# Kernel tuning notes

Measured on AMD Instinct MI355X. Metric: run time of the kernel, lower is better.

## Reference

```python
import jax, jax.numpy as jnp
import numpy as np

TAU = 2.0   # spikingjelly LIFNode default tau
VTH = 1.0   # config.vthreshold

@jax.custom_vjp
def atan_spike(x):
    # heaviside forward, ATan surrogate backward (spikingjelly surrogate.ATan, alpha=2)
    return (x >= 0).astype(x.dtype)

def _atan_fwd(x):
    return atan_spike(x), x

def _atan_bwd(x, g):
    alpha = 2.0
    return (g * (alpha / 2.0) / (1.0 + (jnp.pi / 2.0 * alpha * x) ** 2),)

atan_spike.defvjp(_atan_fwd, _atan_bwd)

def layer_norm(x, eps=1e-6):
    m = jnp.mean(x, axis=-1, keepdims=True)
    v = jnp.mean((x - m) ** 2, axis=-1, keepdims=True)
    return (x - m) * jax.lax.rsqrt(v + eps)

def time_shift(x):
    # ZeroPad2d((0,0,1,-1)): xx[:, t] = x[:, t-1], xx[:, 0] = 0
    return jnp.pad(x, ((0, 0), (1, 0), (0, 0)))[:, :-1]

def lif_multistep(x4):
    # spikingjelly LIFNode, step_mode='m', decay_input=True, hard reset to v_reset=0
    def step(v, xt):
        v = v + (xt - v) / TAU
        s = atan_spike(v - VTH)
        return v * (1.0 - s), s
    _, spikes = jax.lax.scan(step, jnp.zeros_like(x4[0]), x4)
    return spikes

def wkv(w, u, k, v):
    # RWKV-v4 numerically-stable WKV scan. w: [C] (negative), u: [C], k,v: [B,T,C]
    B, T, C = k.shape
    def step(carry, kv):
        aa, bb, pp = carry
        kt, vt = kv
        ww = u + kt
        p = jnp.maximum(pp, ww)
        e1 = jnp.exp(pp - p); e2 = jnp.exp(ww - p)
        y = (e1 * aa + e2 * vt) / (e1 * bb + e2)
        ww2 = pp + w
        p2 = jnp.maximum(ww2, kt)
        f1 = jnp.exp(ww2 - p2); f2 = jnp.exp(kt - p2)
        return (f1 * aa + f2 * vt, f1 * bb + f2, p2), y
    init = (jnp.zeros((B, C), k.dtype), jnp.zeros((B, C), k.dtype),
            jnp.full((B, C), -1e38, k.dtype))
    _, ys = jax.lax.scan(step, init, (jnp.moveaxis(k, 1, 0), jnp.moveaxis(v, 1, 0)))
    return jnp.moveaxis(ys, 0, 1)

def time_mix(h, time_decay, time_first, tmk, tmv, tmr, Wk, Wv, Wr, Wo):
    xx = time_shift(h)
    xk = h * tmk + xx * (1 - tmk)
    xv = h * tmv + xx * (1 - tmv)
    xr = h * tmr + xx * (1 - tmr)
    k = jnp.einsum('btc,oc->bto', xk, Wk)
    v = jnp.einsum('btc,oc->bto', xv, Wv)
    sr = jax.nn.sigmoid(jnp.einsum('btc,oc->bto', xr, Wr))
    y = wkv(-jnp.exp(time_decay), time_first, k, v)
    return jnp.einsum('btc,oc->bto', sr * y, Wo)

def channel_mix(h, cmk, cmr, Wck, Wcv, Wcr):
    xx = time_shift(h)
    xk = h * cmk + xx * (1 - cmk)
    xr = h * cmr + xx * (1 - cmr)
    k = jnp.square(jax.nn.relu(jnp.einsum('btc,hc->bth', xk, Wck)))
    kv = jnp.einsum('bth,ch->btc', k, Wcv)
    return jax.nn.sigmoid(jnp.einsum('btc,oc->bto', xr, Wcr)) * kv

def _forward(x, rt, time_decay, time_first, tmix_k, tmix_v, tmix_r,
             Wk, Wv, Wr, Wo, cmix_k, cmix_r, Wck, Wcv, Wcr,
             Wrm, brm, Wam, bam):
    B, P1, C = x.shape
    xc = jnp.concatenate([x, jnp.broadcast_to(rt, (B, P1, C))], axis=1)  # [B, 2*P1, C]
    att = time_mix(layer_norm(xc), time_decay, time_first,
                   tmix_k, tmix_v, tmix_r, Wk, Wv, Wr, Wo)
    att = lif_multistep(jnp.broadcast_to(att, (4,) + att.shape)).mean(0)
    xc = xc + att
    ffn = channel_mix(layer_norm(xc), cmix_k, cmix_r, Wck, Wcv, Wcr)
    ffn = lif_multistep(jnp.broadcast_to(ffn, (4,) + ffn.shape)).mean(0)
    xc = xc + ffn
    xo, rtok = xc[:, :P1], xc[:, P1:]
    r = jnp.einsum('bpc,qc->bpq', rtok, Wrm) + brm   # restruction_token_MLP [B,P1,P1]
    r = jnp.swapaxes(r, 1, 2)                        # permute(0,2,1)
    r = jnp.einsum('bpq,cq->bpc', r, Wam) + bam      # another_MLP [B,P1,C]
    return xo + xo * r

def setup_inputs() -> dict:
    key = jax.random.key(0)
    ks = jax.random.split(key, 20)
    B, P1, C = 8, 256, 1024
    H = 4 * C
    s = 0.02
    f32 = jnp.float32
    return {
        'x': jax.random.normal(ks[0], (B, P1, C), f32),
        'rt': jax.random.normal(ks[1], (1, P1, C), f32) * 0.5,
        'time_decay': jax.random.normal(ks[2], (C,), f32),
        'time_first': jax.random.normal(ks[3], (C,), f32) * 0.3,
        'tmix_k': jax.random.uniform(ks[4], (1, 1, C), f32),
        'tmix_v': jax.random.uniform(ks[5], (1, 1, C), f32),
        'tmix_r': jax.random.uniform(ks[6], (1, 1, C), f32),
        'Wk': jax.random.normal(ks[7], (C, C), f32) * s,
        'Wv': jax.random.normal(ks[8], (C, C), f32) * s,
        'Wr': jax.random.normal(ks[9], (C, C), f32) * s,
        'Wo': jax.random.normal(ks[10], (C, C), f32) * s,
        'cmix_k': jax.random.uniform(ks[11], (1, 1, C), f32),
        'cmix_r': jax.random.uniform(ks[12], (1, 1, C), f32),
        'Wck': jax.random.normal(ks[13], (H, C), f32) * s,
        'Wcv': jax.random.normal(ks[14], (C, H), f32) * s,
        'Wcr': jax.random.normal(ks[15], (C, C), f32) * s,
        'Wrm': jax.random.normal(ks[16], (P1, C), f32) * s,
        'brm': jax.random.normal(ks[17], (P1,), f32) * s,
        'Wam': jax.random.normal(ks[18], (C, P1), f32) * s,
        'bam': jax.random.normal(ks[19], (C,), f32) * s,
    }

def reference(x, rt, time_decay, time_first, tmix_k, tmix_v, tmix_r,
              Wk, Wv, Wr, Wo, cmix_k, cmix_r, Wck, Wcv, Wcr,
              Wrm, brm, Wam, bam):
    return _forward(x, rt, time_decay, time_first, tmix_k, tmix_v, tmix_r,
                    Wk, Wv, Wr, Wo, cmix_k, cmix_r, Wck, Wcv, Wcr,
                    Wrm, brm, Wam, bam)
```

## Files before the change

### kernel.cpp

```cpp
#include <hip/hip_runtime.h>
#include <hip/hip_bf16.h>
#include <math.h>
#include <stdint.h>

#define TB_ 8
#define TT_ 512
#define TC_ 1024
#define WKV_NCH 32
#define WKV_L 16

typedef __attribute__((ext_vector_type(8))) short bf16x8;
typedef __attribute__((ext_vector_type(4))) short s16x4;
typedef __attribute__((ext_vector_type(4))) float f32x4;

__device__ __forceinline__ float b2f(short u) {
  union { unsigned int i; float f; } x;
  x.i = ((unsigned int)(unsigned short)u) << 16;
  return x.f;
}
__device__ __forceinline__ short f2b(float f) {
  __hip_bfloat16 h = __float2bfloat16(f);
  return __builtin_bit_cast(short, h);
}
__device__ __forceinline__ float sigm(float x) { return 1.0f / (1.0f + expf(-x)); }

__device__ __forceinline__ float lif4(float a) {
  float v = 0.0f, acc = 0.0f;
#pragma unroll
  for (int i = 0; i < 4; ++i) {
    v += (a - v) * 0.5f;
    float s = (v >= 1.0f) ? 1.0f : 0.0f;
    acc += s;
    v *= (1.0f - s);
  }
  return acc * 0.25f;
}

__device__ __forceinline__ void gload16(const void* g, void* l) {
  __builtin_amdgcn_global_load_lds(
      (__attribute__((address_space(1))) void*)(g),
      (__attribute__((address_space(3))) void*)(l), 16, 0, 0);
}

template <int N>
__device__ __forceinline__ void waitv() {
  if constexpr (N == 0)  asm volatile("s_waitcnt vmcnt(0)" ::: "memory");
  else if constexpr (N == 2)  asm volatile("s_waitcnt vmcnt(2)" ::: "memory");
  else if constexpr (N == 4)  asm volatile("s_waitcnt vmcnt(4)" ::: "memory");
  else if constexpr (N == 8)  asm volatile("s_waitcnt vmcnt(8)" ::: "memory");
  else if constexpr (N == 12) asm volatile("s_waitcnt vmcnt(12)" ::: "memory");
  else if constexpr (N == 16) asm volatile("s_waitcnt vmcnt(16)" ::: "memory");
  else if constexpr (N == 20) asm volatile("s_waitcnt vmcnt(20)" ::: "memory");
  else if constexpr (N == 24) asm volatile("s_waitcnt vmcnt(24)" ::: "memory");
  else if constexpr (N == 28) asm volatile("s_waitcnt vmcnt(28)" ::: "memory");
  else static_assert(N == 0, "unsupported vmcnt");
}
__device__ __forceinline__ void barrier_() {
  asm volatile("s_barrier" ::: "memory");
}


__global__ __launch_bounds__(256) void ln_mix3(
    const float* __restrict__ x, const float* __restrict__ rt,
    const float* __restrict__ tmk, const float* __restrict__ tmv,
    const float* __restrict__ tmr, float* __restrict__ xc,
    short* __restrict__ xk, short* __restrict__ xv, short* __restrict__ xr) {
  __shared__ float red[256];
  int row = blockIdx.x;
  int t = row & 511, b = row >> 9;
  int tid = threadIdx.x;
  const float* src = (t < 256) ? x + (int64_t)(b * 256 + t) * TC_
                               : rt + (int64_t)(t - 256) * TC_;
  float4 v = ((const float4*)src)[tid];
  ((float4*)(xc + (int64_t)row * TC_))[tid] = v;
  red[tid] = v.x + v.y + v.z + v.w;
  __syncthreads();
  for (int off = 128; off > 0; off >>= 1) {
    if (tid < off) red[tid] += red[tid + off];
    __syncthreads();
  }
  float mean = red[0] * (1.0f / 1024.0f);
  __syncthreads();
  float dx = v.x - mean, dy = v.y - mean, dz = v.z - mean, dw = v.w - mean;
  red[tid] = dx * dx + dy * dy + dz * dz + dw * dw;
  __syncthreads();
  for (int off = 128; off > 0; off >>= 1) {
    if (tid < off) red[tid] += red[tid + off];
    __syncthreads();
  }
  float rs = 1.0f / sqrtf(red[0] * (1.0f / 1024.0f) + 1e-6f);
  float c0 = dx * rs, c1 = dy * rs, c2 = dz * rs, c3 = dw * rs;
  float p0 = 0.f, p1 = 0.f, p2 = 0.f, p3 = 0.f;
  if (t > 0) {
    int tp = t - 1;
    const float* srcp = (tp < 256) ? x + (int64_t)(b * 256 + tp) * TC_
                                   : rt + (int64_t)(tp - 256) * TC_;
    __syncthreads();
    float4 w4 = ((const float4*)srcp)[tid];
    red[tid] = w4.x + w4.y + w4.z + w4.w;
    __syncthreads();
    for (int off = 128; off > 0; off >>= 1) {
      if (tid < off) red[tid] += red[tid + off];
      __syncthreads();
    }
    float meanp = red[0] * (1.0f / 1024.0f);
    __syncthreads();
    float ex = w4.x - meanp, ey = w4.y - meanp, ez = w4.z - meanp,
          ew = w4.w - meanp;
    red[tid] = ex * ex + ey * ey + ez * ez + ew * ew;
    __syncthreads();
    for (int off = 128; off > 0; off >>= 1) {
      if (tid < off) red[tid] += red[tid + off];
      __syncthreads();
    }
    float rsp = 1.0f / sqrtf(red[0] * (1.0f / 1024.0f) + 1e-6f);
    p0 = ex * rsp; p1 = ey * rsp; p2 = ez * rsp; p3 = ew * rsp;
  }
  int c = tid * 4;
  int64_t o = (int64_t)row * TC_ + c;
  float m0, m1, m2, m3;
  s16x4 ov;
  m0 = tmk[c]; m1 = tmk[c + 1]; m2 = tmk[c + 2]; m3 = tmk[c + 3];
  ov.x = f2b(c0 * m0 + p0 * (1.0f - m0));
  ov.y = f2b(c1 * m1 + p1 * (1.0f - m1));
  ov.z = f2b(c2 * m2 + p2 * (1.0f - m2));
  ov.w = f2b(c3 * m3 + p3 * (1.0f - m3));
  *(s16x4*)(xk + o) = ov;
  m0 = tmv[c]; m1 = tmv[c + 1]; m2 = tmv[c + 2]; m3 = tmv[c + 3];
  ov.x = f2b(c0 * m0 + p0 * (1.0f - m0));
  ov.y = f2b(c1 * m1 + p1 * (1.0f - m1));
  ov.z = f2b(c2 * m2 + p2 * (1.0f - m2));
  ov.w = f2b(c3 * m3 + p3 * (1.0f - m3));
  *(s16x4*)(xv + o) = ov;
  m0 = tmr[c]; m1 = tmr[c + 1]; m2 = tmr[c + 2]; m3 = tmr[c + 3];
  ov.x = f2b(c0 * m0 + p0 * (1.0f - m0));
  ov.y = f2b(c1 * m1 + p1 * (1.0f - m1));
  ov.z = f2b(c2 * m2 + p2 * (1.0f - m2));
  ov.w = f2b(c3 * m3 + p3 * (1.0f - m3));
  *(s16x4*)(xr + o) = ov;
}

__global__ __launch_bounds__(256) void ln_mix2(const float* __restrict__ xc,
                                               const float* __restrict__ cmk,
                                               const float* __restrict__ cmr,
                                               short* __restrict__ xk,
                                               short* __restrict__ xr) {
  __shared__ float red[256];
  int row = blockIdx.x;
  int t = row & 511;
  int tid = threadIdx.x;
  float4 v = ((const float4*)(xc + (int64_t)row * TC_))[tid];
  red[tid] = v.x + v.y + v.z + v.w;
  __syncthreads();
  for (int off = 128; off > 0; off >>= 1) {
    if (tid < off) red[tid] += red[tid + off];
    __syncthreads();
  }
  float mean = red[0] * (1.0f / 1024.0f);
  __syncthreads();
  float dx = v.x - mean, dy = v.y - mean, dz = v.z - mean, dw = v.w - mean;
  red[tid] = dx * dx + dy * dy + dz * dz + dw * dw;
  __syncthreads();
  for (int off = 128; off > 0; off >>= 1) {
    if (tid < off) red[tid] += red[tid + off];
    __syncthreads();
  }
  float rs = 1.0f / sqrtf(red[0] * (1.0f / 1024.0f) + 1e-6f);
  float c0 = dx * rs, c1 = dy * rs, c2 = dz * rs, c3 = dw * rs;
  float p0 = 0.f, p1 = 0.f, p2 = 0.f, p3 = 0.f;
  if (t > 0) {
    __syncthreads();
    float4 w4 = ((const float4*)(xc + (int64_t)(row - 1) * TC_))[tid];
    red[tid] = w4.x + w4.y + w4.z + w4.w;
    __syncthreads();
    for (int off = 128; off > 0; off >>= 1) {
      if (tid < off) red[tid] += red[tid + off];
      __syncthreads();
    }
    float meanp = red[0] * (1.0f / 1024.0f);
    __syncthreads();
    float ex = w4.x - meanp, ey = w4.y - meanp, ez = w4.z - meanp,
          ew = w4.w - meanp;
    red[tid] = ex * ex + ey * ey + ez * ez + ew * ew;
    __syncthreads();
    for (int off = 128; off > 0; off >>= 1) {
      if (tid < off) red[tid] += red[tid + off];
      __syncthreads();
    }
    float rsp = 1.0f / sqrtf(red[0] * (1.0f / 1024.0f) + 1e-6f);
    p0 = ex * rsp; p1 = ey * rsp; p2 = ez * rsp; p3 = ew * rsp;
  }
  int c = tid * 4;
  float k0 = cmk[c], k1 = cmk[c + 1], k2 = cmk[c + 2], k3 = cmk[c + 3];
  float r0 = cmr[c], r1 = cmr[c + 1], r2 = cmr[c + 2], r3 = cmr[c + 3];
  s16x4 ok, orr;
  ok.x = f2b(c0 * k0 + p0 * (1.0f - k0));
  ok.y = f2b(c1 * k1 + p1 * (1.0f - k1));
  ok.z = f2b(c2 * k2 + p2 * (1.0f - k2));
  ok.w = f2b(c3 * k3 + p3 * (1.0f - k3));
  orr.x = f2b(c0 * r0 + p0 * (1.0f - r0));
  orr.y = f2b(c1 * r1 + p1 * (1.0f - r1));
  orr.z = f2b(c2 * r2 + p2 * (1.0f - r2));
  orr.w = f2b(c3 * r3 + p3 * (1.0f - r3));
  *(s16x4*)(xk + (int64_t)row * TC_ + c) = ok;
  *(s16x4*)(xr + (int64_t)row * TC_ + c) = orr;
}

__global__ __launch_bounds__(256) void cvt_b(const float* __restrict__ src,
                                             short* __restrict__ dst) {
  int64_t i = (int64_t)(blockIdx.x * 256 + threadIdx.x) * 8;
  float4 a = *(const float4*)(src + i);
  float4 b = *(const float4*)(src + i + 4);
  bf16x8 o;
  o[0] = f2b(a.x); o[1] = f2b(a.y); o[2] = f2b(a.z); o[3] = f2b(a.w);
  o[4] = f2b(b.x); o[5] = f2b(b.y); o[6] = f2b(b.z); o[7] = f2b(b.w);
  *(bf16x8*)(dst + i) = o;
}

__global__ __launch_bounds__(256) void cvt_all(
    const float* __restrict__ Wk, const float* __restrict__ Wv,
    const float* __restrict__ Wr, const float* __restrict__ Wo,
    const float* __restrict__ Wcr, const float* __restrict__ Wcv,
    const float* __restrict__ Wrm, const float* __restrict__ Wam,
    short* __restrict__ bWk, short* __restrict__ bWv, short* __restrict__ bWr,
    short* __restrict__ bWo, short* __restrict__ bWcr, short* __restrict__ bWcv,
    short* __restrict__ bWrm, short* __restrict__ bWam,
    float* __restrict__ S) {
  int bid = blockIdx.x;
  if (bid >= 4864) {
    int row = (bid - 4864) * 4 + (threadIdx.x >> 6);
    int lane = threadIdx.x & 63;
    float4 v = ((const float4*)(Wam + (int64_t)row * 256))[lane];
    float s = v.x + v.y + v.z + v.w;
    for (int off = 32; off > 0; off >>= 1) s += __shfl_down(s, off);
    if (lane == 0) S[row] = s;
    return;
  }
  const float* src; short* dst; int base;
  if (bid < 512)       { src = Wk;  dst = bWk;  base = bid; }
  else if (bid < 1024) { src = Wv;  dst = bWv;  base = bid - 512; }
  else if (bid < 1536) { src = Wr;  dst = bWr;  base = bid - 1024; }
  else if (bid < 2048) { src = Wo;  dst = bWo;  base = bid - 1536; }
  else if (bid < 2560) { src = Wcr; dst = bWcr; base = bid - 2048; }
  else if (bid < 4608) { src = Wcv; dst = bWcv; base = bid - 2560; }
  else if (bid < 4736) { src = Wrm; dst = bWrm; base = bid - 4608; }
  else                 { src = Wam; dst = bWam; base = bid - 4736; }
  int64_t i = ((int64_t)base * 256 + threadIdx.x) * 8;
  float4 a = *(const float4*)(src + i);
  float4 b = *(const float4*)(src + i + 4);
  bf16x8 o;
  o[0] = f2b(a.x); o[1] = f2b(a.y); o[2] = f2b(a.z); o[3] = f2b(a.w);
  o[4] = f2b(b.x); o[5] = f2b(b.y); o[6] = f2b(b.z); o[7] = f2b(b.w);
  *(bf16x8*)(dst + i) = o;
}

__global__ __launch_bounds__(256) void wkv_p1(const float* __restrict__ td,
                                              const short* __restrict__ K,
                                              const short* __restrict__ V,
                                              float* __restrict__ Ca,
                                              float* __restrict__ Da,
                                              float* __restrict__ Qa) {
  int bx = blockIdx.x;
  int ch = bx >> 5;
  int b = (bx >> 2) & 7;
  int c = (bx & 3) * 256 + threadIdx.x;
  float w = -expf(td[c]);
  float aa = 0.0f, bb = 0.0f, pp = -1e38f;
  int64_t base = ((int64_t)b * TT_ + ch * WKV_L) * TC_ + c;
#pragma unroll
  for (int t = 0; t < WKV_L; ++t) {
    int64_t o = base + (int64_t)t * TC_;
    float kt = b2f(K[o]), vt = b2f(V[o]);
    float ww2 = pp + w;
    float p2 = fmaxf(ww2, kt);
    float e1 = expf(ww2 - p2);
    float e2 = expf(kt - p2);
    aa = e1 * aa + e2 * vt;
    bb = e1 * bb + e2;
    pp = p2;
  }
  int idx = ch * 8192 + b * 1024 + c;
  Ca[idx] = aa; Da[idx] = bb; Qa[idx] = pp;
}

__global__ __launch_bounds__(256) void wkv_p2(const float* __restrict__ td,
                                              const float* __restrict__ Ca,
                                              const float* __restrict__ Da,
                                              const float* __restrict__ Qa,
                                              float* __restrict__ Aa,
                                              float* __restrict__ Ba,
                                              float* __restrict__ Pa) {
  int i = blockIdx.x * 256 + threadIdx.x;
  int c = i & (TC_ - 1);
  float wL = -expf(td[c]) * (float)WKV_L;
  float aa = 0.0f, bb = 0.0f, pp = -1e38f;
#pragma unroll 4
  for (int ch = 0; ch < WKV_NCH; ++ch) {
    int idx = ch * 8192 + i;
    Aa[idx] = aa; Ba[idx] = bb; Pa[idx] = pp;
    float ppw = pp + wL;
    float q = Qa[idx];
    float p2 = fmaxf(ppw, q);
    float ea = expf(ppw - p2);
    float eb = expf(q - p2);
    aa = aa * ea + Ca[idx] * eb;
    bb = bb * ea + Da[idx] * eb;
    pp = p2;
  }
}

__global__ __launch_bounds__(256) void wkv_p3(const float* __restrict__ td,
                                              const float* __restrict__ tf,
                                              const short* __restrict__ K,
                                              const short* __restrict__ V,
                                              const short* __restrict__ SR,
                                              short* __restrict__ SRY,
                                              const float* __restrict__ Aa,
                                              const float* __restrict__ Ba,
                                              const float* __restrict__ Pa) {
  int bx = blockIdx.x;
  int ch = bx >> 5;
  int b = (bx >> 2) & 7;
  int c = (bx & 3) * 256 + threadIdx.x;
  float w = -expf(td[c]);
  float u = tf[c];
  int idx = ch * 8192 + b * 1024 + c;
  float aa = Aa[idx], bb = Ba[idx], pp = Pa[idx];
  int64_t base = ((int64_t)b * TT_ + ch * WKV_L) * TC_ + c;
#pragma unroll
  for (int t = 0; t < WKV_L; ++t) {
    int64_t o = base + (int64_t)t * TC_;
    float kt = b2f(K[o]), vt = b2f(V[o]);
    float ww = u + kt;
    float p = fmaxf(pp, ww);
    float E1 = expf(pp - p);
    float E2 = expf(ww - p);
    float y = (E1 * aa + E2 * vt) / (E1 * bb + E2);
    SRY[o] = f2b(y * b2f(SR[o]));
    float ww2 = pp + w;
    float p2 = fmaxf(ww2, kt);
    float e1 = expf(ww2 - p2);
    float e2 = expf(kt - p2);
    aa = e1 * aa + e2 * vt;
    bb = e1 * bb + e2;
    pp = p2;
  }
}

template <int BM, int BN, int EPI, int D, int MINW>
__global__ __launch_bounds__(256, MINW) void gemm_bf16(
    const short* __restrict__ A, const short* __restrict__ B,
    void* __restrict__ Cp, int M, int N, int K, int Kst,
    int64_t sA, int64_t sB, int64_t sC,
    const float* __restrict__ e0, const float* __restrict__ e1,
    const float* __restrict__ e2, const void* __restrict__ e3, int64_t sE) {
  constexpr int MF = BM / 32;
  constexpr int NF = BN / 32;
  constexpr int ASLOT = BM / 64;
  constexpr int BSLOT = BN / 64;
  constexpr int NL = ASLOT + BSLOT;
  constexpr int SBUF = (BM + BN) * 32;
  __shared__ short lds[D * SBUF];
  const int tid = threadIdx.x;

  const unsigned gx = gridDim.x, gy = gridDim.y;
  const unsigned nwg = gx * gy * gridDim.z;
  const unsigned lin = blockIdx.x + gx * (blockIdx.y + gy * blockIdx.z);
  const unsigned cs = nwg >> 3;
  const unsigned nl = (lin & 7) * cs + (lin >> 3);
  const unsigned bxs = nl % gx;
  const unsigned tmp = nl / gx;
  const unsigned bys = tmp % gy;
  const unsigned bz = tmp / gy;

  const int brow = bys * BM;
  const int bcol = bxs * BN;
  const short* Ab = A + bz * sA;
  const short* Bb = B + bz * sB;

  const int srow = ((tid >> 6) << 4) + (tid & 15);
  const int skc = ((tid >> 4) & 3) * 8;
  const short* gA[ASLOT];
  const short* gB[BSLOT];
#pragma unroll
  for (int s = 0; s < ASLOT; ++s)
    gA[s] = Ab + (int64_t)(brow + s * 64 + srow) * Kst + skc;
#pragma unroll
  for (int s = 0; s < BSLOT; ++s)
    gB[s] = Bb + (int64_t)(bcol + s * 64 + srow) * Kst + skc;

  const int lane = tid & 63, wid = tid >> 6;
  const int wr = wid >> 1, wc = wid & 1;

  f32x4 acc[MF][NF] = {};

  auto stage = [&](int buf, int k0) {
    short* d = lds + buf * SBUF;
#pragma unroll
    for (int s = 0; s < ASLOT; ++s)
      gload16(gA[s] + k0, d + s * 2048 + tid * 8);
#pragma unroll
    for (int s = 0; s < BSLOT; ++s)
      gload16(gB[s] + k0, d + BM * 32 + s * 2048 + tid * 8);
  };
  auto compute = [&](int buf) {
    const short* base = lds + buf * SBUF;
    bf16x8 af[MF], bfv[NF];
#pragma unroll
    for (int m = 0; m < MF; ++m)
      af[m] = *(const bf16x8*)(base + (wr * MF + m) * 512 + lane * 8);
#pragma unroll
    for (int n = 0; n < NF; ++n)
      bfv[n] = *(const bf16x8*)(base + BM * 32 + (wc * NF + n) * 512 + lane * 8);
#pragma unroll
    for (int m = 0; m < MF; ++m)
#pragma unroll
      for (int n = 0; n < NF; ++n)
        acc[m][n] = __builtin_amdgcn_mfma_f32_16x16x32_bf16(af[m], bfv[n],
                                                            acc[m][n], 0, 0, 0);
  };

  const int nst = K / 32;
#pragma unroll
  for (int d = 0; d < D - 1; ++d) stage(d, d * 32);
  for (int t = 0; t <= nst - D; ++t) {
    stage((t + D - 1) & (D - 1), (t + D - 1) * 32);
    waitv<(D - 1) * NL>();
    barrier_();
    compute(t & (D - 1));
    barrier_();
  }
  {
    int t = nst - D + 1;
    if constexpr (D >= 8) {
      waitv<6 * NL>(); barrier_(); compute(t & (D - 1)); barrier_(); ++t;
      waitv<5 * NL>(); barrier_(); compute(t & (D - 1)); barrier_(); ++t;
      waitv<4 * NL>(); barrier_(); compute(t & (D - 1)); barrier_(); ++t;
      waitv<3 * NL>(); barrier_(); compute(t & (D - 1)); barrier_(); ++t;
    }
    if constexpr (D >= 4) {
      waitv<2 * NL>(); barrier_(); compute(t & (D - 1)); barrier_(); ++t;
      waitv<1 * NL>(); barrier_(); compute(t & (D - 1)); barrier_(); ++t;
    }
    waitv<0>(); barrier_(); compute(t & (D - 1));
  }

  const int r0 = brow + wr * (BM / 2) + (lane >> 4) * 4;
  const int c0 = bcol + wc * (BN / 2) + (lane & 15);
#pragma unroll
  for (int m = 0; m < MF; ++m) {
#pragma unroll
    for (int j = 0; j < 4; ++j) {
      int row = r0 + m * 16 + j;
#pragma unroll
      for (int n = 0; n < NF; ++n) {
        int col = c0 + n * 16;
        float v = acc[m][n][j];
        int64_t idx = (int64_t)row * N + col;
        if (EPI == 0) {
          ((short*)Cp)[bz * sC + idx] = f2b(v);
        } else if (EPI == 1) {
          ((short*)Cp)[bz * sC + idx] = f2b(sigm(v));
        } else if (EPI == 2) {
          v = fmaxf(v, 0.0f);
          ((short*)Cp)[bz * sC + idx] = f2b(v * v);
        } else if (EPI == 3) {
          float r2 = v + e0[row] * e1[col] + e2[col];
          float xo = ((const float*)e3)[bz * sE + idx];
          ((float*)Cp)[bz * sC + idx] = xo * (1.0f + r2);
        } else if (EPI == 4) {
          float* XC = (float*)Cp;
          XC[idx] = XC[idx] + lif4(v);
        } else if (EPI == 5) {
          float* XC = (float*)Cp;
          float srr = b2f(((const short*)e3)[idx]);
          float nv = XC[idx] + lif4(v * srr);
          XC[idx] = nv;
          int tt = row & 511;
          if (tt >= 256) {
            short* rtok = (short*)(void*)const_cast<float*>(e1);
            rtok[(((int64_t)(row >> 9)) * 256 + (tt - 256)) * 1024 + col] =
                f2b(nv);
          }
        } else if (EPI == 6) {
          ((short*)Cp)[bz * sC + idx] = f2b(bz == 2 ? sigm(v) : v);
        }
      }
    }
  }
}

extern "C" void kernel_launch(void* const* d_in, const int* in_sizes, int n_in,
                              void* d_out, int out_size, void* d_ws,
                              size_t ws_size, hipStream_t stream) {
  const float* x   = (const float*)d_in[0];
  const float* rt  = (const float*)d_in[1];
  const float* td  = (const float*)d_in[2];
  const float* tf  = (const float*)d_in[3];
  const float* tmk = (const float*)d_in[4];
  const float* tmv = (const float*)d_in[5];
  const float* tmr = (const float*)d_in[6];
  const float* Wk  = (const float*)d_in[7];
  const float* Wv  = (const float*)d_in[8];
  const float* Wr  = (const float*)d_in[9];
  const float* Wo  = (const float*)d_in[10];
  const float* cmk = (const float*)d_in[11];
  const float* cmr = (const float*)d_in[12];
  const float* Wck = (const float*)d_in[13];
  const float* Wcv = (const float*)d_in[14];
  const float* Wcr = (const float*)d_in[15];
  const float* Wrm = (const float*)d_in[16];
  const float* brm = (const float*)d_in[17];
  const float* Wam = (const float*)d_in[18];
  const float* bam = (const float*)d_in[19];
  float* out = (float*)d_out;

  const size_t MB = 1ull << 20;
  uint8_t* W8 = (uint8_t*)d_ws;
  float* XC   = (float*)(W8);
  short* S1   = (short*)(W8 + 24 * MB);
  short* S2   = (short*)(W8 + 32 * MB);
  short* S3   = (short*)(W8 + 40 * MB);
  short* bWcv = (short*)(W8 + 48 * MB);
  short* bWk  = (short*)(W8 + 56 * MB);
  short* bWo  = (short*)(W8 + 62 * MB);
  short* bWcr = (short*)(W8 + 64 * MB);
  short* bWrm = (short*)(W8 + 66 * MB);
  short* bWam = (short*)(W8 + 66 * MB + 512 * 1024);
  short* KK   = (short*)(W8 + 67 * MB);
  short* VV   = (short*)(W8 + 75 * MB);
  short* RR   = (short*)(W8 + 83 * MB);
  float* Ca   = (float*)(W8 + 91 * MB);
  float* Da   = (float*)(W8 + 92 * MB);
  float* Qa   = (float*)(W8 + 93 * MB);
  float* Aa   = (float*)(W8 + 94 * MB);
  float* Ba   = (float*)(W8 + 95 * MB);
  float* Pa   = (float*)(W8 + 96 * MB);
  short* SRY  = S1;
  short* xk2  = S2;
  short* xr2  = S3;
  short* SRR  = S1;
  short* bWck = S3;
  short* H16  = KK;
  short* rtok = S2;
  short* Mt   = (short*)(W8 + 36 * MB);
  float* Sb   = (float*)(W8 + 99 * MB);

  dim3 blk(256);

  cvt_all<<<5120, blk, 0, stream>>>(Wk, Wv, Wr, Wo, Wcr, Wcv, Wrm, Wam,
                                    bWk, bWk + 1048576, bWk + 2097152, bWo,
                                    bWcr, bWcv, bWrm, bWam, Sb);

  ln_mix3<<<TB_ * TT_, blk, 0, stream>>>(x, rt, tmk, tmv, tmr, XC, S1, S2, S3);

  gemm_bf16<128, 128, 6, 2, 3><<<dim3(8, 32, 3), blk, 0, stream>>>(
      S1, bWk, KK, 4096, 1024, 1024, 1024, 4194304, 1048576, 4194304,
      nullptr, nullptr, nullptr, nullptr, 0);
  wkv_p1<<<WKV_NCH * TB_ * 4, blk, 0, stream>>>(td, KK, VV, Ca, Da, Qa);
  wkv_p2<<<32, blk, 0, stream>>>(td, Ca, Da, Qa, Aa, Ba, Pa);
  wkv_p3<<<WKV_NCH * TB_ * 4, blk, 0, stream>>>(td, tf, KK, VV, RR, SRY,
                                                Aa, Ba, Pa);
  gemm_bf16<128, 128, 4, 8, 1><<<dim3(8, 32, 1), blk, 0, stream>>>(
      SRY, bWo, XC, 4096, 1024, 1024, 1024, 0, 0, 0,
      nullptr, nullptr, nullptr, nullptr, 0);
  ln_mix2<<<TB_ * TT_, blk, 0, stream>>>(XC, cmk, cmr, xk2, xr2);
  gemm_bf16<128, 128, 1, 8, 1><<<dim3(8, 32, 1), blk, 0, stream>>>(
      xr2, bWcr, SRR, 4096, 1024, 1024, 1024, 0, 0, 0,
      nullptr, nullptr, nullptr, nullptr, 0);
  cvt_b<<<2048, blk, 0, stream>>>(Wck, bWck);
  gemm_bf16<128, 128, 2, 2, 4><<<dim3(32, 32, 1), blk, 0, stream>>>(
      xk2, bWck, H16, 4096, 4096, 1024, 1024, 0, 0, 0,
      nullptr, nullptr, nullptr, nullptr, 0);
  gemm_bf16<128, 128, 5, 8, 1><<<dim3(8, 32, 1), blk, 0, stream>>>(
      H16, bWcv, XC, 4096, 1024, 4096, 4096, 0, 0, 0,
      nullptr, (const float*)rtok, nullptr, SRR, 0);
  gemm_bf16<64, 64, 0, 2, 2><<<dim3(4, 4, 8), blk, 0, stream>>>(
      bWrm, rtok, Mt, 256, 256, 1024, 1024, 0, (int64_t)256 * 1024,
      (int64_t)256 * 256, nullptr, nullptr, nullptr, nullptr, 0);
  gemm_bf16<64, 64, 3, 2, 2><<<dim3(16, 4, 8), blk, 0, stream>>>(
      Mt, bWam, out, 256, 1024, 256, 256, (int64_t)256 * 256, 0,
      (int64_t)256 * 1024, brm, Sb, bam, XC, (int64_t)512 * 1024);
}
```

Baseline: 342.8 us.

## Add 512-thread double-buffered GEMM for N=1024 projections and split rtok conversion

Adds a new 512-thread, 8-wave GEMM kernel with a 128x128 tile, K=64 steps and double-buffered LDS. It interleaves the direct-to-LDS global loads with MFMA work in half-steps. This kernel replaces the deep-pipeline (D=8) 256-thread GEMMs for the output projection, the channel-mix receptance and the value projection, aiming for more waves per tile and better latency hiding on these 256-block grids. The bf16 rtok scatter moves out of the GEMM epilogue into a separate conversion kernel, which adds one launch and an extra read of XC.

```diff
diff --git a/kernel.cpp b/kernel.cpp
--- a/kernel.cpp
+++ b/kernel.cpp
@@ -49,10 +49,6 @@
   else if constexpr (N == 4)  asm volatile("s_waitcnt vmcnt(4)" ::: "memory");
   else if constexpr (N == 8)  asm volatile("s_waitcnt vmcnt(8)" ::: "memory");
   else if constexpr (N == 12) asm volatile("s_waitcnt vmcnt(12)" ::: "memory");
-  else if constexpr (N == 16) asm volatile("s_waitcnt vmcnt(16)" ::: "memory");
-  else if constexpr (N == 20) asm volatile("s_waitcnt vmcnt(20)" ::: "memory");
-  else if constexpr (N == 24) asm volatile("s_waitcnt vmcnt(24)" ::: "memory");
-  else if constexpr (N == 28) asm volatile("s_waitcnt vmcnt(28)" ::: "memory");
   else static_assert(N == 0, "unsupported vmcnt");
 }
 __device__ __forceinline__ void barrier_() {
@@ -215,6 +211,20 @@
   o[0] = f2b(a.x); o[1] = f2b(a.y); o[2] = f2b(a.z); o[3] = f2b(a.w);
   o[4] = f2b(b.x); o[5] = f2b(b.y); o[6] = f2b(b.z); o[7] = f2b(b.w);
   *(bf16x8*)(dst + i) = o;
+}
+
+__global__ __launch_bounds__(256) void cvt_rtok(const float* __restrict__ xc,
+                                                short* __restrict__ dst) {
+  int i = blockIdx.x * 256 + threadIdx.x;
+  int b = i >> 15;
+  int rem = i & 32767;
+  const float* s = xc + (int64_t)b * 524288 + 262144 + (int64_t)rem * 8;
+  float4 a = *(const float4*)s;
+  float4 c = *(const float4*)(s + 4);
+  bf16x8 o;
+  o[0] = f2b(a.x); o[1] = f2b(a.y); o[2] = f2b(a.z); o[3] = f2b(a.w);
+  o[4] = f2b(c.x); o[5] = f2b(c.y); o[6] = f2b(c.z); o[7] = f2b(c.w);
+  *(bf16x8*)(dst + (int64_t)i * 8) = o;
 }
 
 __global__ __launch_bounds__(256) void cvt_all(
@@ -347,6 +357,125 @@
   }
 }
 
+template <int EPI>
+__global__ __launch_bounds__(512, 1) void gemm4p(
+    const short* __restrict__ A, const short* __restrict__ B,
+    void* __restrict__ Cp, int M, int N, int K, int Kst,
+    const float* __restrict__ e0, const float* __restrict__ e1,
+    const float* __restrict__ e2, const void* __restrict__ e3) {
+  __shared__ short lds[2 * 32768];
+  const int tid = threadIdx.x;
+
+  const unsigned gx = gridDim.x, gy = gridDim.y;
+  const unsigned nwg = gx * gy;
+  const unsigned lin = blockIdx.x + gx * blockIdx.y;
+  const unsigned cs = nwg >> 3;
+  const unsigned nl = (lin & 7) * cs + (lin >> 3);
+  const unsigned bxs = nl % gx;
+  const unsigned bys = nl / gx;
+
+  const int brow = bys * 128;
+  const int bcol = bxs * 128;
+
+  const int srow = ((tid >> 6) << 4) + (tid & 15);
+  const int skc = ((tid >> 4) & 3) * 8;
+  const short* gA = A + (int64_t)(brow + srow) * Kst + skc;
+  const short* gB = B + (int64_t)(bcol + srow) * Kst + skc;
+
+  const int lane = tid & 63, wid = tid >> 6;
+  const int wr = wid >> 2, wc = wid & 3;
+
+  f32x4 acc[4][2] = {};
+
+#define RD_A(rb, kh, m) \
+  (*(const bf16x8*)(lds + (rb) * 32768 + (kh) * 8192 + (wr * 4 + (m)) * 512 + lane * 8))
+#define RD_B(rb, kh, n) \
+  (*(const bf16x8*)(lds + (rb) * 32768 + 16384 + (kh) * 8192 + (wc * 2 + (n)) * 512 + lane * 8))
+#define ST_A(sb, kh, kt) \
+  gload16(gA + (kt) * 64 + (kh) * 32, lds + (sb) * 32768 + (kh) * 8192 + tid * 8)
+#define ST_B(sb, kh, kt) \
+  gload16(gB + (kt) * 64 + (kh) * 32, lds + (sb) * 32768 + 16384 + (kh) * 8192 + tid * 8)
+#define MM(am, bn, i, j) \
+  acc[i][j] = __builtin_amdgcn_mfma_f32_16x16x32_bf16(am, bn, acc[i][j], 0, 0, 0)
+
+  const int nt = K / 64;
+  ST_A(0, 0, 0); ST_B(0, 0, 0); ST_A(0, 1, 0); ST_B(0, 1, 0);
+  waitv<2>();
+  barrier_();
+
+  for (int t = 0; t < nt - 1; ++t) {
+    const int rb = t & 1, sb = rb ^ 1, kn = t + 1;
+    {
+      bf16x8 a0 = RD_A(rb, 0, 0), a1 = RD_A(rb, 0, 1);
+      bf16x8 b0 = RD_B(rb, 0, 0), b1 = RD_B(rb, 0, 1);
+      ST_A(sb, 0, kn);
+      MM(a0, b0, 0, 0); MM(a0, b1, 0, 1); MM(a1, b0, 1, 0); MM(a1, b1, 1, 1);
+      barrier_();
+      bf16x8 a2 = RD_A(rb, 0, 2), a3 = RD_A(rb, 0, 3);
+      ST_B(sb, 0, kn);
+      MM(a2, b0, 2, 0); MM(a2, b1, 2, 1); MM(a3, b0, 3, 0); MM(a3, b1, 3, 1);
+      waitv<2>();
+      barrier_();
+    }
+    {
+      bf16x8 a0 = RD_A(rb, 1, 0), a1 = RD_A(rb, 1, 1);
+      bf16x8 b0 = RD_B(rb, 1, 0), b1 = RD_B(rb, 1, 1);
+      ST_A(sb, 1, kn);
+      MM(a0, b0, 0, 0); MM(a0, b1, 0, 1); MM(a1, b0, 1, 0); MM(a1, b1, 1, 1);
+      barrier_();
+      bf16x8 a2 = RD_A(rb, 1, 2), a3 = RD_A(rb, 1, 3);
+      ST_B(sb, 1, kn);
+      MM(a2, b0, 2, 0); MM(a2, b1, 2, 1); MM(a3, b0, 3, 0); MM(a3, b1, 3, 1);
+      waitv<2>();
+      barrier_();
+    }
+  }
+  {
+    waitv<0>();
+    barrier_();
+    const int rb = (nt - 1) & 1;
+#pragma unroll
+    for (int kh = 0; kh < 2; ++kh) {
+      bf16x8 a0 = RD_A(rb, kh, 0), a1 = RD_A(rb, kh, 1);
+      bf16x8 a2 = RD_A(rb, kh, 2), a3 = RD_A(rb, kh, 3);
+      bf16x8 b0 = RD_B(rb, kh, 0), b1 = RD_B(rb, kh, 1);
+      MM(a0, b0, 0, 0); MM(a0, b1, 0, 1); MM(a1, b0, 1, 0); MM(a1, b1, 1, 1);
+      MM(a2, b0, 2, 0); MM(a2, b1, 2, 1); MM(a3, b0, 3, 0); MM(a3, b1, 3, 1);
+    }
+  }
+#undef RD_A
+#undef RD_B
+#undef ST_A
+#undef ST_B
+#undef MM
+
+  const int r0 = brow + wr * 64 + (lane >> 4) * 4;
+  const int c0 = bcol + wc * 32 + (lane & 15);
+#pragma unroll
+  for (int m = 0; m < 4; ++m) {
+#pragma unroll
+    for (int j = 0; j < 4; ++j) {
+      int row = r0 + m * 16 + j;
+#pragma unroll
+      for (int n = 0; n < 2; ++n) {
+        int col = c0 + n * 16;
+        float v = acc[m][n][j];
+        int64_t idx = (int64_t)row * N + col;
+        if (EPI == 1) {
+          ((short*)Cp)[idx] = f2b(sigm(v));
+        } else if (EPI == 4) {
+          float* XC = (float*)Cp;
+          XC[idx] = XC[idx] + lif4(v);
+        } else if (EPI == 5) {
+          float* XC = (float*)Cp;
+          float srr = b2f(((const short*)e3)[idx]);
+          XC[idx] = XC[idx] + lif4(v * srr);
+        }
+      }
+    }
+  }
+}
+
 template <int BM, int BN, int EPI, int D, int MINW>
 __global__ __launch_bounds__(256, MINW) void gemm_bf16(
     const short* __restrict__ A, const short* __restrict__ B,
@@ -432,12 +561,6 @@
   }
   {
     int t = nst - D + 1;
-    if constexpr (D >= 8) {
-      waitv<6 * NL>(); barrier_(); compute(t & (D - 1)); barrier_(); ++t;
-      waitv<5 * NL>(); barrier_(); compute(t & (D - 1)); barrier_(); ++t;
-      waitv<4 * NL>(); barrier_(); compute(t & (D - 1)); barrier_(); ++t;
-      waitv<3 * NL>(); barrier_(); compute(t & (D - 1)); barrier_(); ++t;
-    }
     if constexpr (D >= 4) {
       waitv<2 * NL>(); barrier_(); compute(t & (D - 1)); barrier_(); ++t;
       waitv<1 * NL>(); barrier_(); compute(t & (D - 1)); barrier_(); ++t;
@@ -459,8 +582,6 @@
         int64_t idx = (int64_t)row * N + col;
         if (EPI == 0) {
           ((short*)Cp)[bz * sC + idx] = f2b(v);
-        } else if (EPI == 1) {
-          ((short*)Cp)[bz * sC + idx] = f2b(sigm(v));
         } else if (EPI == 2) {
           v = fmaxf(v, 0.0f);
           ((short*)Cp)[bz * sC + idx] = f2b(v * v);
@@ -468,20 +589,6 @@
           float r2 = v + e0[row] * e1[col] + e2[col];
           float xo = ((const float*)e3)[bz * sE + idx];
           ((float*)Cp)[bz * sC + idx] = xo * (1.0f + r2);
-        } else if (EPI == 4) {
-          float* XC = (float*)Cp;
-          XC[idx] = XC[idx] + lif4(v);
-        } else if (EPI == 5) {
-          float* XC = (float*)Cp;
-          float srr = b2f(((const short*)e3)[idx]);
-          float nv = XC[idx] + lif4(v * srr);
-          XC[idx] = nv;
-          int tt = row & 511;
-          if (tt >= 256) {
-            short* rtok = (short*)(void*)const_cast<float*>(e1);
-            rtok[(((int64_t)(row >> 9)) * 256 + (tt - 256)) * 1024 + col] =
-                f2b(nv);
-          }
         } else if (EPI == 6) {
           ((short*)Cp)[bz * sC + idx] = f2b(bz == 2 ? sigm(v) : v);
         }
@@ -547,6 +654,7 @@
   float* Sb   = (float*)(W8 + 99 * MB);
 
   dim3 blk(256);
+  dim3 blk512(512);
 
   cvt_all<<<5120, blk, 0, stream>>>(Wk, Wv, Wr, Wo, Wcr, Wcv, Wrm, Wam,
                                     bWk, bWk + 1048576, bWk + 2097152, bWo,
@@ -561,20 +669,20 @@
   wkv_p2<<<32, blk, 0, stream>>>(td, Ca, Da, Qa, Aa, Ba, Pa);
   wkv_p3<<<WKV_NCH * TB_ * 4, blk, 0, stream>>>(td, tf, KK, VV, RR, SRY,
                                                 Aa, Ba, Pa);
-  gemm_bf16<128, 128, 4, 8, 1><<<dim3(8, 32, 1), blk, 0, stream>>>(
-      SRY, bWo, XC, 4096, 1024, 1024, 1024, 0, 0, 0,
-      nullptr, nullptr, nullptr, nullptr, 0);
+  gemm4p<4><<<dim3(8, 32), blk512, 0, stream>>>(
+      SRY, bWo, XC, 4096, 1024, 1024, 1024, nullptr, nullptr, nullptr,
+      nullptr);
   ln_mix2<<<TB_ * TT_, blk, 0, stream>>>(XC, cmk, cmr, xk2, xr2);
-  gemm_bf16<128, 128, 1, 8, 1><<<dim3(8, 32, 1), blk, 0, stream>>>(
-      xr2, bWcr, SRR, 4096, 1024, 1024, 1024, 0, 0, 0,
-      nullptr, nullptr, nullptr, nullptr, 0);
+  gemm4p<1><<<dim3(8, 32), blk512, 0, stream>>>(
+      xr2, bWcr, SRR, 4096, 1024, 1024, 1024, nullptr, nullptr, nullptr,
+      nullptr);
   cvt_b<<<2048, blk, 0, stream>>>(Wck, bWck);
   gemm_bf16<128, 128, 2, 2, 4><<<dim3(32, 32, 1), blk, 0, stream>>>(
       xk2, bWck, H16, 4096, 4096, 1024, 1024, 0, 0, 0,
       nullptr, nullptr, nullptr, nullptr, 0);
-  gemm_bf16<128, 128, 5, 8, 1><<<dim3(8, 32, 1), blk, 0, stream>>>(
-      H16, bWcv, XC, 4096, 1024, 4096, 4096, 0, 0, 0,
-      nullptr, (const float*)rtok, nullptr, SRR, 0);
+  gemm4p<5><<<dim3(8, 32), blk512, 0, stream>>>(
+      H16, bWcv, XC, 4096, 1024, 4096, 4096, nullptr, nullptr, nullptr, SRR);
+  cvt_rtok<<<1024, blk, 0, stream>>>(XC, rtok);
   gemm_bf16<64, 64, 0, 2, 2><<<dim3(4, 4, 8), blk, 0, stream>>>(
       bWrm, rtok, Mt, 256, 256, 1024, 1024, 0, (int64_t)256 * 1024,
       (int64_t)256 * 256, nullptr, nullptr, nullptr, nullptr, 0);
```

After: 328.6 us. 1.04x faster.
